# Performance work log

Measured on AMD Instinct MI355X. Metric: run time of the kernel, lower is better.

The kernel has to match this reference:

```python
import jax, jax.numpy as jnp
import numpy as np

NEG_SLOPE = 0.01  # torch nn.LeakyReLU default


def setup_inputs() -> dict:
    key = jax.random.key(0)
    k1, k2, k3, k4 = jax.random.split(key, 4)
    N, D_IN, D_OUT = 8192, 200, 128
    H = jax.random.normal(k1, (N, D_IN), dtype=jnp.float32)
    A = jax.random.normal(k2, (N, N), dtype=jnp.float32)
    W = jax.random.normal(k3, (D_IN, D_OUT), dtype=jnp.float32) * (1.0 / np.sqrt(D_IN))
    b = jax.random.normal(k4, (D_OUT,), dtype=jnp.float32) * 0.01
    return {"H": H, "A": A, "W": W, "b": b}


def reference(H, A, W, b):
    # A = clamp(sigmoid(A), min=0.1)
    A = jnp.maximum(jax.nn.sigmoid(A), 0.1)
    # D^-1/2 A D^-1/2 -- diag matmuls are equivalent to row/col broadcast scaling
    d_inv_sqrt = jnp.power(A.sum(axis=1), -0.5)  # [N]
    A_hat = A * d_inv_sqrt[:, None] * d_inv_sqrt[None, :]
    # Linear then aggregate
    HW = H @ W + b  # [N, D_OUT]
    out = A_hat @ HW
    out = jnp.where(out >= 0, out, NEG_SLOPE * out)  # LeakyReLU
    return out, A
```

## Files before the change

kernel.cpp:

```cpp
#include <hip/hip_runtime.h>
#include <hip/hip_bf16.h>

#define NR 8192
#define DIN 200
#define DOUT 128

typedef __attribute__((ext_vector_type(8))) short short8;
typedef __attribute__((ext_vector_type(4))) float f32x4;

__device__ __forceinline__ unsigned short f2bf(float x) {
    union { float f; unsigned u; } v; v.f = x;
    unsigned r = v.u + 0x7FFFu + ((v.u >> 16) & 1u);
    return (unsigned short)(r >> 16);
}

__device__ __forceinline__ float4 sig4(float4 x) {
    float4 s;
    s.x = fmaxf(__builtin_amdgcn_rcpf(1.f + __expf(-x.x)), 0.1f);
    s.y = fmaxf(__builtin_amdgcn_rcpf(1.f + __expf(-x.y)), 0.1f);
    s.z = fmaxf(__builtin_amdgcn_rcpf(1.f + __expf(-x.z)), 0.1f);
    s.w = fmaxf(__builtin_amdgcn_rcpf(1.f + __expf(-x.w)), 0.1f);
    return s;
}

__global__ __launch_bounds__(256) void k_sum(const float* __restrict__ A,
                                             float* __restrict__ dis) {
    const int row = blockIdx.x;
    const float4* __restrict__ ar = (const float4*)(A + (size_t)row * NR);
    float sum = 0.f;
#pragma unroll
    for (int i = 0; i < 8; ++i) {
        float4 s = sig4(ar[i * 256 + threadIdx.x]);
        sum += (s.x + s.y) + (s.z + s.w);
    }
#pragma unroll
    for (int off = 32; off > 0; off >>= 1) sum += __shfl_down(sum, off, 64);
    __shared__ float red[4];
    if ((threadIdx.x & 63) == 0) red[threadIdx.x >> 6] = sum;
    __syncthreads();
    if (threadIdx.x == 0)
        dis[row] = __builtin_amdgcn_rsqf((red[0] + red[1]) + (red[2] + red[3]));
}

__global__ __launch_bounds__(256) void k_vt(const float* __restrict__ H,
                                            const float* __restrict__ W,
                                            const float* __restrict__ bias,
                                            const float* __restrict__ dis,
                                            unsigned short* __restrict__ VT) {
    __shared__ float hs[32 * 201];
    const int rowBase = blockIdx.x * 32;
    for (int i = threadIdx.x; i < 32 * DIN; i += 256) {
        int r = i / DIN;
        int k = i - r * DIN;
        hs[r * 201 + k] = H[(size_t)rowBase * DIN + i];
    }
    __syncthreads();
    const int c0 = (threadIdx.x & 31) * 4;
    const int rg = threadIdx.x >> 5;
    float acc[4][4];
#pragma unroll
    for (int r = 0; r < 4; ++r)
#pragma unroll
        for (int i = 0; i < 4; ++i) acc[r][i] = 0.f;
#pragma unroll 4
    for (int k = 0; k < DIN; ++k) {
        float4 w4 = *(const float4*)(W + k * DOUT + c0);
#pragma unroll
        for (int r = 0; r < 4; ++r) {
            float h = hs[(rg * 4 + r) * 201 + k];
            acc[r][0] = fmaf(h, w4.x, acc[r][0]);
            acc[r][1] = fmaf(h, w4.y, acc[r][1]);
            acc[r][2] = fmaf(h, w4.z, acc[r][2]);
            acc[r][3] = fmaf(h, w4.w, acc[r][3]);
        }
    }
    float4 b4 = *(const float4*)(bias + c0);
    float bb[4] = {b4.x, b4.y, b4.z, b4.w};
    float dsc[4];
#pragma unroll
    for (int r = 0; r < 4; ++r) dsc[r] = dis[rowBase + rg * 4 + r];
#pragma unroll
    for (int i = 0; i < 4; ++i) {
        ushort4 pk;
        pk.x = f2bf(dsc[0] * (acc[0][i] + bb[i]));
        pk.y = f2bf(dsc[1] * (acc[1][i] + bb[i]));
        pk.z = f2bf(dsc[2] * (acc[2][i] + bb[i]));
        pk.w = f2bf(dsc[3] * (acc[3][i] + bb[i]));
        *(ushort4*)(VT + (size_t)(c0 + i) * NR + rowBase + rg * 4) = pk;
    }
}

#define BK 32
#define LDK 40
#define NIT 128

__global__ __launch_bounds__(256) void k_gemm(const float* __restrict__ A,
                                              const unsigned short* __restrict__ VT,
                                              float* __restrict__ A2,
                                              float* __restrict__ P) {
    __shared__ alignas(16) unsigned short lA[2][32 * LDK];
    __shared__ alignas(16) unsigned short lV[2][128 * LDK];
    const int tid = threadIdx.x;
    const int blockRow = blockIdx.x & 255;
    const int s = blockIdx.x >> 8;
    const int rowBase = blockRow * 32;
    const size_t kb0 = (size_t)s * 4096;

    const int am = tid >> 3, ak = (tid & 7) * 4;
    const size_t aoff = (size_t)(rowBase + am) * NR + kb0 + ak;
    const float* __restrict__ ap = A + aoff;
    float* __restrict__ a2p = A2 + aoff;
    const int vc = tid >> 2, vq = (tid & 3) * 8;
    const unsigned short* __restrict__ vp0 = VT + (size_t)vc * NR + kb0 + vq;
    const unsigned short* __restrict__ vp1 = vp0 + (size_t)64 * NR;

    const int lane = tid & 63, w = tid >> 6;
    const int rt = w & 1, cg = w >> 1;
    const int fm = lane & 15, kq = lane >> 4;

    f32x4 acc[4];
#pragma unroll
    for (int nt = 0; nt < 4; ++nt) {
        acc[nt][0] = 0.f; acc[nt][1] = 0.f; acc[nt][2] = 0.f; acc[nt][3] = 0.f;
    }

    float4 ga, gv0, gv1;

    ga  = *(const float4*)(ap);
    gv0 = *(const float4*)(vp0);
    gv1 = *(const float4*)(vp1);
    {
        float4 sg = sig4(ga);
        *(float4*)(a2p) = sg;
        ushort4 pa; pa.x = f2bf(sg.x); pa.y = f2bf(sg.y); pa.z = f2bf(sg.z); pa.w = f2bf(sg.w);
        *(ushort4*)(&lA[0][am * LDK + ak]) = pa;
        *(float4*)(&lV[0][vc * LDK + vq]) = gv0;
        *(float4*)(&lV[0][(vc + 64) * LDK + vq]) = gv1;
    }
    ga  = *(const float4*)(ap + BK);
    gv0 = *(const float4*)(vp0 + BK);
    gv1 = *(const float4*)(vp1 + BK);

    const unsigned short* lap = &lA[0][(rt * 16 + fm) * LDK + kq * 8];
    const unsigned short* lvp = &lV[0][(cg * 64 + fm) * LDK + kq * 8];
    const int strideA = 32 * LDK;
    const int strideV = 128 * LDK;

    for (int i = 0; i < NIT; ++i) {
        __syncthreads();
        if (i + 1 < NIT) {
            const int nb = (i + 1) & 1;
            float4 sg = sig4(ga);
            *(float4*)(a2p + (size_t)(i + 1) * BK) = sg;
            ushort4 pa; pa.x = f2bf(sg.x); pa.y = f2bf(sg.y); pa.z = f2bf(sg.z); pa.w = f2bf(sg.w);
            *(ushort4*)(&lA[nb][am * LDK + ak]) = pa;
            *(float4*)(&lV[nb][vc * LDK + vq]) = gv0;
            *(float4*)(&lV[nb][(vc + 64) * LDK + vq]) = gv1;
        }
        if (i + 2 < NIT) {
            const size_t off = (size_t)(i + 2) * BK;
            ga  = *(const float4*)(ap + off);
            gv0 = *(const float4*)(vp0 + off);
            gv1 = *(const float4*)(vp1 + off);
        }
        const int cb = i & 1;
        short8 a8 = *(const short8*)(lap + cb * strideA);
#pragma unroll
        for (int nt = 0; nt < 4; ++nt) {
            short8 b8 = *(const short8*)(lvp + cb * strideV + nt * 16 * LDK);
            acc[nt] = __builtin_amdgcn_mfma_f32_16x16x32_bf16(a8, b8, acc[nt], 0, 0, 0);
        }
    }

    float* __restrict__ Pp = P + (size_t)s * ((size_t)NR * DOUT);
    const int row0 = rowBase + rt * 16 + kq * 4;
    const int col0 = cg * 64 + fm;
#pragma unroll
    for (int nt = 0; nt < 4; ++nt) {
#pragma unroll
        for (int v = 0; v < 4; ++v) {
            Pp[(size_t)(row0 + v) * DOUT + col0 + nt * 16] = acc[nt][v];
        }
    }
}

__global__ __launch_bounds__(256) void k_comb(const float* __restrict__ P,
                                              const float* __restrict__ dis,
                                              float* __restrict__ out) {
    const int idx = blockIdx.x * 256 + threadIdx.x;
    const float d = dis[idx >> 5];
    const float4 p0 = *(const float4*)(P + (size_t)idx * 4);
    const float4 p1 = *(const float4*)(P + (size_t)idx * 4 + (size_t)NR * DOUT);
    float4 o;
    o.x = d * (p0.x + p1.x); o.x = o.x >= 0.f ? o.x : 0.01f * o.x;
    o.y = d * (p0.y + p1.y); o.y = o.y >= 0.f ? o.y : 0.01f * o.y;
    o.z = d * (p0.z + p1.z); o.z = o.z >= 0.f ? o.z : 0.01f * o.z;
    o.w = d * (p0.w + p1.w); o.w = o.w >= 0.f ? o.w : 0.01f * o.w;
    *(float4*)(out + (size_t)idx * 4) = o;
}

extern "C" void kernel_launch(void* const* d_in, const int* in_sizes, int n_in,
                              void* d_out, int out_size, void* d_ws, size_t ws_size,
                              hipStream_t stream) {
    const float* H = (const float*)d_in[0];
    const float* A = (const float*)d_in[1];
    const float* W = (const float*)d_in[2];
    const float* b = (const float*)d_in[3];

    float* out = (float*)d_out;
    float* A2  = out + (size_t)NR * DOUT;

    char* ws = (char*)d_ws;
    float* dis = (float*)ws;
    unsigned short* VT = (unsigned short*)(ws + 65536);
    float* P = (float*)(ws + (4u << 20));

    k_sum <<<NR,   256, 0, stream>>>(A, dis);
    k_vt  <<<256,  256, 0, stream>>>(H, W, b, dis, VT);
    k_gemm<<<512,  256, 0, stream>>>(A, VT, A2, P);
    k_comb<<<1024, 256, 0, stream>>>(P, dis, out);
}
```

Before: 588.0 us.

## Precompute bf16 sigmoid matrix in row-sum pass and split GEMM K four ways

The row-sum kernel now writes the clamped sigmoid output (A2) and a bf16 copy of it, so the GEMM reads a 2-byte operand and no longer recomputes sigmoid or writes A2. The K dimension is split four ways instead of two, giving 1024 GEMM blocks, and the combine kernel sums four partial slices. This removes a second fp32 read of the 256MB A matrix and the transcendental work from the GEMM. In exchange it adds a 128MB bf16 write and read, plus larger partial buffers to reduce.

New measurement: 527.3 us. 10.3% less time.

```diff
diff --git a/kernel.cpp b/kernel.cpp
--- a/kernel.cpp
+++ b/kernel.cpp
@@ -5,8 +5,16 @@
 #define DIN 200
 #define DOUT 128
 
+#define NSPLIT 4
+#define KSPL 2048
+#define BK 32
+#define LDK 40
+#define NIT 64
+
 typedef __attribute__((ext_vector_type(8))) short short8;
 typedef __attribute__((ext_vector_type(4))) float f32x4;
+typedef __attribute__((ext_vector_type(4))) float fv4;
+typedef __attribute__((ext_vector_type(4))) unsigned short u16x4;
 
 __device__ __forceinline__ unsigned short f2bf(float x) {
     union { float f; unsigned u; } v; v.f = x;
@@ -14,24 +22,34 @@
     return (unsigned short)(r >> 16);
 }
 
-__device__ __forceinline__ float4 sig4(float4 x) {
-    float4 s;
-    s.x = fmaxf(__builtin_amdgcn_rcpf(1.f + __expf(-x.x)), 0.1f);
-    s.y = fmaxf(__builtin_amdgcn_rcpf(1.f + __expf(-x.y)), 0.1f);
-    s.z = fmaxf(__builtin_amdgcn_rcpf(1.f + __expf(-x.z)), 0.1f);
-    s.w = fmaxf(__builtin_amdgcn_rcpf(1.f + __expf(-x.w)), 0.1f);
+__device__ __forceinline__ fv4 sig4(fv4 x) {
+    fv4 s;
+    s[0] = fmaxf(__builtin_amdgcn_rcpf(1.f + __expf(-x[0])), 0.1f);
+    s[1] = fmaxf(__builtin_amdgcn_rcpf(1.f + __expf(-x[1])), 0.1f);
+    s[2] = fmaxf(__builtin_amdgcn_rcpf(1.f + __expf(-x[2])), 0.1f);
+    s[3] = fmaxf(__builtin_amdgcn_rcpf(1.f + __expf(-x[3])), 0.1f);
     return s;
 }
 
 __global__ __launch_bounds__(256) void k_sum(const float* __restrict__ A,
+                                             float* __restrict__ A2,
+                                             unsigned short* __restrict__ SA,
                                              float* __restrict__ dis) {
     const int row = blockIdx.x;
-    const float4* __restrict__ ar = (const float4*)(A + (size_t)row * NR);
+    const fv4* __restrict__ ar = (const fv4*)(A + (size_t)row * NR);
+    fv4* __restrict__ a2r = (fv4*)(A2 + (size_t)row * NR);
+    u16x4* __restrict__ sar = (u16x4*)(SA + (size_t)row * NR);
     float sum = 0.f;
 #pragma unroll
     for (int i = 0; i < 8; ++i) {
-        float4 s = sig4(ar[i * 256 + threadIdx.x]);
-        sum += (s.x + s.y) + (s.z + s.w);
+        const int idx = i * 256 + threadIdx.x;
+        fv4 x = __builtin_nontemporal_load(&ar[idx]);
+        fv4 s = sig4(x);
+        __builtin_nontemporal_store(s, &a2r[idx]);
+        u16x4 pk;
+        pk[0] = f2bf(s[0]); pk[1] = f2bf(s[1]); pk[2] = f2bf(s[2]); pk[3] = f2bf(s[3]);
+        sar[idx] = pk;
+        sum += (s[0] + s[1]) + (s[2] + s[3]);
     }
 #pragma unroll
     for (int off = 32; off > 0; off >>= 1) sum += __shfl_down(sum, off, 64);
@@ -90,26 +108,19 @@
     }
 }
 
-#define BK 32
-#define LDK 40
-#define NIT 128
-
-__global__ __launch_bounds__(256) void k_gemm(const float* __restrict__ A,
-                                              const unsigned short* __restrict__ VT,
-                                              float* __restrict__ A2,
-                                              float* __restrict__ P) {
+__global__ __launch_bounds__(256, 4) void k_gemm(const unsigned short* __restrict__ SA,
+                                                 const unsigned short* __restrict__ VT,
+                                                 float* __restrict__ P) {
     __shared__ alignas(16) unsigned short lA[2][32 * LDK];
     __shared__ alignas(16) unsigned short lV[2][128 * LDK];
     const int tid = threadIdx.x;
     const int blockRow = blockIdx.x & 255;
     const int s = blockIdx.x >> 8;
     const int rowBase = blockRow * 32;
-    const size_t kb0 = (size_t)s * 4096;
+    const size_t kb0 = (size_t)s * KSPL;
 
     const int am = tid >> 3, ak = (tid & 7) * 4;
-    const size_t aoff = (size_t)(rowBase + am) * NR + kb0 + ak;
-    const float* __restrict__ ap = A + aoff;
-    float* __restrict__ a2p = A2 + aoff;
+    const unsigned short* __restrict__ ap = SA + (size_t)(rowBase + am) * NR + kb0 + ak;
     const int vc = tid >> 2, vq = (tid & 3) * 8;
     const unsigned short* __restrict__ vp0 = VT + (size_t)vc * NR + kb0 + vq;
     const unsigned short* __restrict__ vp1 = vp0 + (size_t)64 * NR;
@@ -124,22 +135,17 @@
         acc[nt][0] = 0.f; acc[nt][1] = 0.f; acc[nt][2] = 0.f; acc[nt][3] = 0.f;
     }
 
-    float4 ga, gv0, gv1;
-
-    ga  = *(const float4*)(ap);
-    gv0 = *(const float4*)(vp0);
-    gv1 = *(const float4*)(vp1);
-    {
-        float4 sg = sig4(ga);
-        *(float4*)(a2p) = sg;
-        ushort4 pa; pa.x = f2bf(sg.x); pa.y = f2bf(sg.y); pa.z = f2bf(sg.z); pa.w = f2bf(sg.w);
-        *(ushort4*)(&lA[0][am * LDK + ak]) = pa;
-        *(float4*)(&lV[0][vc * LDK + vq]) = gv0;
-        *(float4*)(&lV[0][(vc + 64) * LDK + vq]) = gv1;
-    }
-    ga  = *(const float4*)(ap + BK);
-    gv0 = *(const float4*)(vp0 + BK);
-    gv1 = *(const float4*)(vp1 + BK);
+    u16x4 ga; short8 gv0, gv1;
+
+    ga  = *(const u16x4*)(ap);
+    gv0 = *(const short8*)(vp0);
+    gv1 = *(const short8*)(vp1);
+    *(u16x4*)(&lA[0][am * LDK + ak]) = ga;
+    *(short8*)(&lV[0][vc * LDK + vq]) = gv0;
+    *(short8*)(&lV[0][(vc + 64) * LDK + vq]) = gv1;
+    ga  = *(const u16x4*)(ap + BK);
+    gv0 = *(const short8*)(vp0 + BK);
+    gv1 = *(const short8*)(vp1 + BK);
 
     const unsigned short* lap = &lA[0][(rt * 16 + fm) * LDK + kq * 8];
     const unsigned short* lvp = &lV[0][(cg * 64 + fm) * LDK + kq * 8];
@@ -150,18 +156,15 @@
         __syncthreads();
         if (i + 1 < NIT) {
             const int nb = (i + 1) & 1;
-            float4 sg = sig4(ga);
-            *(float4*)(a2p + (size_t)(i + 1) * BK) = sg;
-            ushort4 pa; pa.x = f2bf(sg.x); pa.y = f2bf(sg.y); pa.z = f2bf(sg.z); pa.w = f2bf(sg.w);
-            *(ushort4*)(&lA[nb][am * LDK + ak]) = pa;
-            *(float4*)(&lV[nb][vc * LDK + vq]) = gv0;
-            *(float4*)(&lV[nb][(vc + 64) * LDK + vq]) = gv1;
+            *(u16x4*)(&lA[nb][am * LDK + ak]) = ga;
+            *(short8*)(&lV[nb][vc * LDK + vq]) = gv0;
+            *(short8*)(&lV[nb][(vc + 64) * LDK + vq]) = gv1;
         }
         if (i + 2 < NIT) {
             const size_t off = (size_t)(i + 2) * BK;
-            ga  = *(const float4*)(ap + off);
-            gv0 = *(const float4*)(vp0 + off);
-            gv1 = *(const float4*)(vp1 + off);
+            ga  = *(const u16x4*)(ap + off);
+            gv0 = *(const short8*)(vp0 + off);
+            gv1 = *(const short8*)(vp1 + off);
         }
         const int cb = i & 1;
         short8 a8 = *(const short8*)(lap + cb * strideA);
@@ -189,14 +192,19 @@
                                               float* __restrict__ out) {
     const int idx = blockIdx.x * 256 + threadIdx.x;
     const float d = dis[idx >> 5];
-    const float4 p0 = *(const float4*)(P + (size_t)idx * 4);
-    const float4 p1 = *(const float4*)(P + (size_t)idx * 4 + (size_t)NR * DOUT);
-    float4 o;
-    o.x = d * (p0.x + p1.x); o.x = o.x >= 0.f ? o.x : 0.01f * o.x;
-    o.y = d * (p0.y + p1.y); o.y = o.y >= 0.f ? o.y : 0.01f * o.y;
-    o.z = d * (p0.z + p1.z); o.z = o.z >= 0.f ? o.z : 0.01f * o.z;
-    o.w = d * (p0.w + p1.w); o.w = o.w >= 0.f ? o.w : 0.01f * o.w;
-    *(float4*)(out + (size_t)idx * 4) = o;
+    const size_t sl = (size_t)NR * DOUT;
+    const fv4 p0 = *(const fv4*)(P + (size_t)idx * 4);
+    const fv4 p1 = *(const fv4*)(P + (size_t)idx * 4 + sl);
+    const fv4 p2 = *(const fv4*)(P + (size_t)idx * 4 + 2 * sl);
+    const fv4 p3 = *(const fv4*)(P + (size_t)idx * 4 + 3 * sl);
+    fv4 t = (p0 + p1) + (p2 + p3);
+    fv4 o;
+#pragma unroll
+    for (int j = 0; j < 4; ++j) {
+        float v = d * t[j];
+        o[j] = v >= 0.f ? v : 0.01f * v;
+    }
+    *(fv4*)(out + (size_t)idx * 4) = o;
 }
 
 extern "C" void kernel_launch(void* const* d_in, const int* in_sizes, int n_in,
@@ -213,10 +221,11 @@
     char* ws = (char*)d_ws;
     float* dis = (float*)ws;
     unsigned short* VT = (unsigned short*)(ws + 65536);
-    float* P = (float*)(ws + (4u << 20));
-
-    k_sum <<<NR,   256, 0, stream>>>(A, dis);
+    float* P = (float*)(ws + (4ull << 20));
+    unsigned short* SA = (unsigned short*)(ws + (20ull << 20));
+
+    k_sum <<<NR,   256, 0, stream>>>(A, A2, SA, dis);
     k_vt  <<<256,  256, 0, stream>>>(H, W, b, dis, VT);
-    k_gemm<<<512,  256, 0, stream>>>(A, VT, A2, P);
+    k_gemm<<<1024, 256, 0, stream>>>(SA, VT, P);
     k_comb<<<1024, 256, 0, stream>>>(P, dis, out);
 }
```
